# Optimization experiments

Hardware: AMD Instinct MI355X
Metric: run time of the kernel (lower is better)

The kernel has to match this reference:

```python
import jax, jax.numpy as jnp
import numpy as np

LEAKY_ALPHA = 0.2  # tf.nn.leaky_relu default


def setup_inputs() -> dict:
    key = jax.random.key(0)
    ks = jax.random.split(key, 8)
    N, F_IN, OUT, E = 100000, 256, 64, 1600000
    x = jax.random.normal(ks[0], (1, N, F_IN), dtype=jnp.float32)
    W = jax.random.normal(ks[1], (F_IN, OUT), dtype=jnp.float32) * 0.05
    a1 = jax.random.normal(ks[2], (OUT, 1), dtype=jnp.float32) * 0.1
    b1 = jnp.zeros((1,), dtype=jnp.float32)
    a2 = jax.random.normal(ks[3], (OUT, 1), dtype=jnp.float32) * 0.1
    b2 = jnp.zeros((1,), dtype=jnp.float32)
    out_bias = jnp.zeros((OUT,), dtype=jnp.float32)
    edge_src = jax.random.randint(ks[4], (E,), 0, N, dtype=jnp.int32)
    edge_dst = jax.random.randint(ks[5], (E,), 0, N, dtype=jnp.int32)
    return {"x": x, "W": W, "a1": a1, "b1": b1, "a2": a2, "b2": b2,
            "out_bias": out_bias, "edge_src": edge_src, "edge_dst": edge_dst,
            "nb_nodes": N}


def reference(x, W, a1, b1, a2, b2, out_bias, edge_src, edge_dst, nb_nodes):
    N = int(nb_nodes)
    h = jnp.einsum('nf,fo->no', x[0], W)          # [N, out_sz] projected features
    f1 = (h @ a1 + b1)[:, 0]                       # [N] per-node src score
    f2 = (h @ a2 + b2)[:, 0]                       # [N] per-node dst score
    # edge logits: f1[src] + f2[dst], leaky relu
    e = jax.nn.leaky_relu(f1[edge_src] + f2[edge_dst], negative_slope=LEAKY_ALPHA)
    # row-wise sparse softmax over edges grouped by src
    m = jax.ops.segment_max(e, edge_src, num_segments=N)
    m = jnp.where(jnp.isfinite(m), m, 0.0)
    ex = jnp.exp(e - m[edge_src])
    denom = jax.ops.segment_sum(ex, edge_src, num_segments=N)
    coefs = ex / denom[edge_src]                   # [E]
    # spmm: aggregate neighbor features
    vals = jax.ops.segment_sum(coefs[:, None] * h[edge_dst], edge_src, num_segments=N)
    ret = jax.nn.elu(vals + out_bias)              # bias_add + elu act
    return ret[None]                               # [1, N, out_sz]
```

## Files before the change

### kernel.cpp

```cpp
#include <hip/hip_runtime.h>
#include <math.h>

#define F_IN 256
#define OUT  64
#define LEAKY 0.2f
#define BSH  9
#define BSZ  512
#define CAP  12288
#define EPB  4096

typedef __attribute__((ext_vector_type(4))) float f32x4;
typedef __attribute__((ext_vector_type(8))) __bf16 bf16x8;
typedef __attribute__((ext_vector_type(4))) unsigned int u32x4;

__device__ __forceinline__ unsigned cvt_pk_bf16(float lo, float hi) {
    unsigned r;
    asm volatile("v_cvt_pk_bf16_f32 %0, %1, %2" : "=v"(r) : "v"(lo), "v"(hi));
    return r;
}

__device__ __forceinline__ float bfl(unsigned u) {
    return __builtin_bit_cast(float, u << 16);
}
__device__ __forceinline__ float bfh(unsigned u) {
    return __builtin_bit_cast(float, u & 0xFFFF0000u);
}

__global__ __launch_bounds__(256) void fused_part_gemm_kernel(
    const float* __restrict__ x, const float* __restrict__ W,
    const float* __restrict__ a1, const float* __restrict__ b1,
    const float* __restrict__ a2, const float* __restrict__ b2,
    unsigned short* __restrict__ h2, float* __restrict__ f1, float* __restrict__ f2,
    const int* __restrict__ esrc, const int* __restrict__ edst,
    int* __restrict__ runstart, int* __restrict__ cntmat, unsigned* __restrict__ ebkt,
    int N, int E, int nPart, int gemmBlocks)
{
    __shared__ __align__(16) unsigned int Wt[64 * 128];
    __shared__ __align__(16) unsigned int xsb[4][2][512];

    const int bid = blockIdx.x;
    const int t   = threadIdx.x;
    const int r   = bid % 3;

    if (r == 2) {
        int c = bid / 3;
        if (c >= nPart) return;
        int* hist = (int*)Wt;
        int* off  = hist + 256;
        int* run  = hist + 512;
        int* sc0  = hist + 768;
        int* sc1  = hist + 1024;
        hist[t] = 0; off[t] = 0;
        __syncthreads();
        const int e0 = c * EPB;
        int ss[16], dd[16], bb[16];
#pragma unroll
        for (int k = 0; k < 4; ++k) {
            int i = e0 + k * 1024 + t * 4;
            if (i + 4 <= E) {
                int4 s4 = *(const int4*)&esrc[i];
                int4 d4 = *(const int4*)&edst[i];
                ss[k * 4 + 0] = s4.x; ss[k * 4 + 1] = s4.y;
                ss[k * 4 + 2] = s4.z; ss[k * 4 + 3] = s4.w;
                dd[k * 4 + 0] = d4.x; dd[k * 4 + 1] = d4.y;
                dd[k * 4 + 2] = d4.z; dd[k * 4 + 3] = d4.w;
#pragma unroll
                for (int q = 0; q < 4; ++q) {
                    bb[k * 4 + q] = ss[k * 4 + q] >> BSH;
                    atomicAdd(&hist[bb[k * 4 + q]], 1);
                }
            } else {
#pragma unroll
                for (int q = 0; q < 4; ++q) {
                    int e = i + q;
                    if (e < E) {
                        ss[k * 4 + q] = esrc[e];
                        dd[k * 4 + q] = edst[e];
                        bb[k * 4 + q] = ss[k * 4 + q] >> BSH;
                        atomicAdd(&hist[bb[k * 4 + q]], 1);
                    } else bb[k * 4 + q] = -1;
                }
            }
        }
        __syncthreads();
        sc0[t] = hist[t];
        __syncthreads();
        int* s = sc0; int* dsts = sc1;
        for (int d = 1; d < 256; d <<= 1) {
            dsts[t] = s[t] + (t >= d ? s[t - d] : 0);
            __syncthreads();
            int* tmp = s; s = dsts; dsts = tmp;
        }
        run[t] = s[t] - hist[t];
        runstart[c * 256 + t] = s[t] - hist[t];
        cntmat [c * 256 + t] = hist[t];
        __syncthreads();
#pragma unroll
        for (int k = 0; k < 16; ++k) {
            if (bb[k] >= 0) {
                int l = atomicAdd(&off[bb[k]], 1);
                ebkt[e0 + run[bb[k]] + l] = (unsigned)dd[k] |
                                            ((unsigned)(ss[k] & (BSZ - 1)) << 17);
            }
        }
        return;
    }

    const int g    = (bid / 3) * 2 + r;
    if (g >= gemmBlocks) return;
    const int wave = t >> 6;
    const int lane = t & 63;
    const int rowB = g * 128;

    for (int p = t; p < 64 * 32; p += 256) {
        int c = p & 63, gg = p >> 6;
        float f[8];
#pragma unroll
        for (int j = 0; j < 8; ++j) f[j] = W[(gg * 8 + j) * 64 + c];
        u32x4 d;
        d.x = cvt_pk_bf16(f[0], f[1]);
        d.y = cvt_pk_bf16(f[2], f[3]);
        d.z = cvt_pk_bf16(f[4], f[5]);
        d.w = cvt_pk_bf16(f[6], f[7]);
        int gs = gg ^ (c & 7);
        *(u32x4*)&Wt[c * 128 + gs * 4] = d;
    }

    const int lrow0 = lane >> 3;
    const int fcol  = (lane & 7) << 2;
    const int sslot = (lane & 7) >> 1;
    const int shalf = (lane & 1) << 1;
    size_t gsrc[4];
    unsigned woff[4];
#pragma unroll
    for (int i = 0; i < 4; ++i) {
        int row  = i * 8 + lrow0;
        int srow = rowB + wave * 32 + row; if (srow > N - 1) srow = N - 1;
        gsrc[i] = (size_t)srow * F_IN + fcol;
        woff[i] = row * 16 + ((sslot ^ (row & 3)) << 2) + shalf;
    }
    unsigned int* xw = &xsb[wave][0][0];

    f32x4 acc[2][4];
#pragma unroll
    for (int m = 0; m < 2; ++m)
#pragma unroll
        for (int n = 0; n < 4; ++n) acc[m][n] = (f32x4){0.f, 0.f, 0.f, 0.f};

    float4 la[4], lb[4];
#pragma unroll
    for (int i = 0; i < 4; ++i) la[i] = *(const float4*)&x[gsrc[i]];

    __syncthreads();

#pragma unroll
    for (int ks = 0; ks < 8; ++ks) {
        const int cur = ks & 1;
        if (ks < 7) {
            const int kc = (ks + 1) * 32;
            if (cur == 0) {
#pragma unroll
                for (int i = 0; i < 4; ++i) lb[i] = *(const float4*)&x[gsrc[i] + kc];
            } else {
#pragma unroll
                for (int i = 0; i < 4; ++i) la[i] = *(const float4*)&x[gsrc[i] + kc];
            }
            asm volatile("s_waitcnt vmcnt(4)" ::: "memory");
        } else {
            asm volatile("s_waitcnt vmcnt(0)" ::: "memory");
        }
        __builtin_amdgcn_sched_barrier(0);

#pragma unroll
        for (int i = 0; i < 4; ++i) {
            float4 v = (cur == 0) ? la[i] : lb[i];
            uint2 w;
            w.x = cvt_pk_bf16(v.x, v.y);
            w.y = cvt_pk_bf16(v.z, v.w);
            *(uint2*)&xw[cur * 512 + woff[i]] = w;
        }

        bf16x8 bfrag[4];
#pragma unroll
        for (int ns = 0; ns < 4; ++ns) {
            int c = ns * 16 + (lane & 15);
            int G = ks * 4 + (lane >> 4);
            u32x4 bw = *(u32x4*)&Wt[c * 128 + ((G ^ (c & 7)) << 2)];
            bfrag[ns] = __builtin_bit_cast(bf16x8, bw);
        }
#pragma unroll
        for (int ms = 0; ms < 2; ++ms) {
            int rr = ms * 16 + (lane & 15);
            int g0 = lane >> 4;
            u32x4 aw = *(u32x4*)&xw[cur * 512 + rr * 16 + ((g0 ^ (rr & 3)) << 2)];
            bf16x8 afrag = __builtin_bit_cast(bf16x8, aw);
#pragma unroll
            for (int ns = 0; ns < 4; ++ns)
                acc[ms][ns] = __builtin_amdgcn_mfma_f32_16x16x32_bf16(afrag, bfrag[ns],
                                                                      acc[ms][ns], 0, 0, 0);
        }
    }

    float A1v[4], A2v[4];
#pragma unroll
    for (int ns = 0; ns < 4; ++ns) {
        A1v[ns] = a1[ns * 16 + (lane & 15)];
        A2v[ns] = a2[ns * 16 + (lane & 15)];
    }
    float B1 = b1[0], B2 = b2[0];
#pragma unroll
    for (int ms = 0; ms < 2; ++ms) {
#pragma unroll
        for (int rr = 0; rr < 4; ++rr) {
            int grow = rowB + wave * 32 + ms * 16 + ((lane >> 4) << 2) + rr;
            float s1 = 0.f, s2 = 0.f;
#pragma unroll
            for (int ns = 0; ns < 4; ++ns) {
                float v = acc[ms][ns][rr];
                if (grow < N)
                    h2[(size_t)grow * OUT + ns * 16 + (lane & 15)] =
                        (unsigned short)(cvt_pk_bf16(v, v) & 0xffffu);
                s1 += v * A1v[ns];
                s2 += v * A2v[ns];
            }
#pragma unroll
            for (int off = 1; off < 16; off <<= 1) {
                s1 += __shfl_xor(s1, off);
                s2 += __shfl_xor(s2, off);
            }
            if ((lane & 15) == 0 && grow < N) { f1[grow] = s1 + B1; f2[grow] = s2 + B2; }
        }
    }
}

__global__ __launch_bounds__(256) void csr_build_kernel(
    const unsigned* __restrict__ ebkt, const int* __restrict__ runstart,
    const int* __restrict__ cntmat,
    int* __restrict__ counts, int* __restrict__ row_start,
    int* __restrict__ csr4, int N, int nPart)
{
    __shared__ int cnt[BSZ];
    __shared__ int cur[BSZ];
    __shared__ int sc[2][BSZ];
    const int b = blockIdx.x;
    const int t = threadIdx.x;

    cnt[t] = 0; cnt[t + 256] = 0;
    __syncthreads();

    for (int c = t; c < nPart; c += 256) {
        int base = c * EPB + runstart[c * 256 + b];
        int n    = cntmat[c * 256 + b];
        for (int i = 0; i < n; ++i)
            atomicAdd(&cnt[ebkt[base + i] >> 17], 1);
    }
    __syncthreads();

    sc[0][t] = cnt[t]; sc[0][t + 256] = cnt[t + 256];
    __syncthreads();
    int srcb = 0;
    for (int d = 1; d < BSZ; d <<= 1) {
        int dstb = srcb ^ 1;
        int i0 = t, i1 = t + 256;
        sc[dstb][i0] = sc[srcb][i0] + (i0 >= d ? sc[srcb][i0 - d] : 0);
        sc[dstb][i1] = sc[srcb][i1] + (i1 >= d ? sc[srcb][i1 - d] : 0);
        __syncthreads();
        srcb = dstb;
    }

    const int nodeBase = b << BSH;
    const int e0out    = b * CAP;
#pragma unroll
    for (int j = 0; j < 2; ++j) {
        int i = t + j * 256;
        int excl = sc[srcb][i] - cnt[i];
        cur[i] = excl;
        int gn = nodeBase + i;
        if (gn < N) {
            row_start[gn] = e0out + excl;
            counts[gn]    = cnt[i];
        }
    }
    __syncthreads();

    for (int c = t; c < nPart; c += 256) {
        int base = c * EPB + runstart[c * 256 + b];
        int n    = cntmat[c * 256 + b];
        for (int i = 0; i < n; ++i) {
            unsigned w = ebkt[base + i];
            int ls = w >> 17;
            int pos = e0out + atomicAdd(&cur[ls], 1);
            csr4[pos] = (int)(w & 0x1FFFFu);
        }
    }
}

__global__ __launch_bounds__(256) void aggregate_kernel(
    const unsigned short* __restrict__ h2, const float* __restrict__ f1,
    const float* __restrict__ f2,
    const int* __restrict__ row_start, const int* __restrict__ counts,
    const int* __restrict__ csr4, const float* __restrict__ out_bias,
    float* __restrict__ out, int N)
{
    const int t    = threadIdx.x;
    const int lane = t & 63;
    const int gl   = lane & 7;
    const int gb   = lane & 56;
    const int gw   = blockIdx.x * 32 + ((t >> 6) << 3) + (lane >> 3);
    if (gw >= N) return;

    const int base  = row_start[gw];
    const int deg   = counts[gw];
    const float f1n = f1[gw];

    float den = 0.f;
    float a[8] = {0.f, 0.f, 0.f, 0.f, 0.f, 0.f, 0.f, 0.f};

    for (int c0 = 0; c0 < deg; c0 += 8) {
        int  idx   = c0 + gl;
        bool valid = idx < deg;
        int   d = valid ? csr4[base + idx] : 0;
        float e = f1n + f2[d];
        e = (e > 0.f) ? e : LEAKY * e;
        float p = valid ? __expf(e) : 0.f;
        den += p;

        unsigned pack = ((unsigned)d << 15) | (cvt_pk_bf16(p, p) & 0x7FFFu);

        int lim = deg - c0; if (lim > 8) lim = 8;
        int j = 0;
        for (; j + 2 <= lim; j += 2) {
            unsigned pk0 = __shfl((int)pack, gb + j);
            unsigned pk1 = __shfl((int)pack, gb + j + 1);
            uint4 u0 = *(const uint4*)&h2[((pk0 >> 15) << 6) + (gl << 3)];
            uint4 u1 = *(const uint4*)&h2[((pk1 >> 15) << 6) + (gl << 3)];
            float p0 = __builtin_bit_cast(float, (pk0 & 0x7FFFu) << 16);
            float p1 = __builtin_bit_cast(float, (pk1 & 0x7FFFu) << 16);
            a[0] += p0 * bfl(u0.x) + p1 * bfl(u1.x);
            a[1] += p0 * bfh(u0.x) + p1 * bfh(u1.x);
            a[2] += p0 * bfl(u0.y) + p1 * bfl(u1.y);
            a[3] += p0 * bfh(u0.y) + p1 * bfh(u1.y);
            a[4] += p0 * bfl(u0.z) + p1 * bfl(u1.z);
            a[5] += p0 * bfh(u0.z) + p1 * bfh(u1.z);
            a[6] += p0 * bfl(u0.w) + p1 * bfl(u1.w);
            a[7] += p0 * bfh(u0.w) + p1 * bfh(u1.w);
        }
        if (j < lim) {
            unsigned pk = __shfl((int)pack, gb + j);
            uint4 u = *(const uint4*)&h2[((pk >> 15) << 6) + (gl << 3)];
            float pp = __builtin_bit_cast(float, (pk & 0x7FFFu) << 16);
            a[0] += pp * bfl(u.x);
            a[1] += pp * bfh(u.x);
            a[2] += pp * bfl(u.y);
            a[3] += pp * bfh(u.y);
            a[4] += pp * bfl(u.z);
            a[5] += pp * bfh(u.z);
            a[6] += pp * bfl(u.w);
            a[7] += pp * bfh(u.w);
        }
    }

    den += __shfl_xor(den, 1);
    den += __shfl_xor(den, 2);
    den += __shfl_xor(den, 4);

    float rd = (deg > 0) ? (1.f / den) : 0.f;
    float4 b0 = *(const float4*)&out_bias[(gl << 3) + 0];
    float4 b1v = *(const float4*)&out_bias[(gl << 3) + 4];
    float v[8];
    v[0] = a[0] * rd + b0.x;  v[1] = a[1] * rd + b0.y;
    v[2] = a[2] * rd + b0.z;  v[3] = a[3] * rd + b0.w;
    v[4] = a[4] * rd + b1v.x; v[5] = a[5] * rd + b1v.y;
    v[6] = a[6] * rd + b1v.z; v[7] = a[7] * rd + b1v.w;
#pragma unroll
    for (int k = 0; k < 8; ++k)
        v[k] = (v[k] > 0.f) ? v[k] : (__expf(v[k]) - 1.f);
    float4 r0 = {v[0], v[1], v[2], v[3]};
    float4 r1 = {v[4], v[5], v[6], v[7]};
    *(float4*)&out[((unsigned)gw << 6) + (gl << 3) + 0] = r0;
    *(float4*)&out[((unsigned)gw << 6) + (gl << 3) + 4] = r1;
}

extern "C" void kernel_launch(void* const* d_in, const int* in_sizes, int n_in,
                              void* d_out, int out_size, void* d_ws, size_t ws_size,
                              hipStream_t stream)
{
    const float* x        = (const float*)d_in[0];
    const float* W        = (const float*)d_in[1];
    const float* a1       = (const float*)d_in[2];
    const float* b1       = (const float*)d_in[3];
    const float* a2       = (const float*)d_in[4];
    const float* b2       = (const float*)d_in[5];
    const float* out_bias = (const float*)d_in[6];
    const int*   esrc     = (const int*)d_in[7];
    const int*   edst     = (const int*)d_in[8];
    const int N = in_sizes[0] / F_IN;
    const int E = in_sizes[7];
    float* out = (float*)d_out;

    char* wsp = (char*)d_ws;
    size_t off = 0;
    auto alloc = [&](size_t bytes) -> void* {
        void* p = wsp + off;
        off = (off + bytes + 255) & ~(size_t)255;
        return p;
    };
    const int nbk   = (N + BSZ - 1) >> BSH;
    const int nPart = (E + EPB - 1) / EPB;

    unsigned short* h2 = (unsigned short*)alloc((size_t)N * OUT * sizeof(unsigned short));
    float* f1          = (float*)alloc((size_t)N * sizeof(float));
    float* f2          = (float*)alloc((size_t)N * sizeof(float));
    int*   counts      = (int*)alloc((size_t)N * sizeof(int));
    int*   row_start   = (int*)alloc((size_t)N * sizeof(int));
    int*   runstart    = (int*)alloc((size_t)nPart * 256 * sizeof(int));
    int*   cntmat      = (int*)alloc((size_t)nPart * 256 * sizeof(int));
    unsigned* ebkt     = (unsigned*)alloc((size_t)nPart * EPB * sizeof(unsigned));
    int*   csr4        = (int*)alloc((size_t)nbk * CAP * sizeof(int));

    const int gemmBlocks = (N + 127) / 128;
    int nGroup = (gemmBlocks + 1) / 2;
    if (nPart > nGroup) nGroup = nPart;

    fused_part_gemm_kernel<<<nGroup * 3, 256, 0, stream>>>(
        x, W, a1, b1, a2, b2, h2, f1, f2, esrc, edst, runstart, cntmat, ebkt,
        N, E, nPart, gemmBlocks);
    csr_build_kernel<<<nbk, 256, 0, stream>>>(ebkt, runstart, cntmat, counts, row_start,
                                              csr4, N, nPart);
    aggregate_kernel<<<(N + 31) / 32, 256, 0, stream>>>(h2, f1, f2, row_start, counts, csr4,
                                                        out_bias, out, N);
}
```

Baseline: 95.47 us.

## Split GEMM across partition and CSR-build kernels to overlap work

The GEMM blocks are now divided between two launches. The first kernel runs the edge partitioning alongside the first G1 GEMM tiles. The second kernel interleaves the CSR build with the remaining GEMM tiles. The aim is to hide the latency-bound CSR build, which has few blocks, behind compute-bound GEMM work, and to balance the first kernel. The split point is a hardcoded constant tuned to this N, and mixing block types may cause load imbalance or shared-memory occupancy limits.

```diff
diff --git a/kernel.cpp b/kernel.cpp
--- a/kernel.cpp
+++ b/kernel.cpp
@@ -8,6 +8,7 @@
 #define BSZ  512
 #define CAP  12288
 #define EPB  4096
+#define G1   586
 
 typedef __attribute__((ext_vector_type(4))) float f32x4;
 typedef __attribute__((ext_vector_type(8))) __bf16 bf16x8;
@@ -24,6 +25,139 @@
 }
 __device__ __forceinline__ float bfh(unsigned u) {
     return __builtin_bit_cast(float, u & 0xFFFF0000u);
+}
+
+__device__ __forceinline__ void gemm_body(
+    int g, int t,
+    const float* __restrict__ x, const float* __restrict__ W,
+    const float* __restrict__ a1, const float* __restrict__ b1,
+    const float* __restrict__ a2, const float* __restrict__ b2,
+    unsigned short* __restrict__ h2, float* __restrict__ f1, float* __restrict__ f2,
+    unsigned int* Wt, unsigned int* xsb, int N)
+{
+    const int wave = t >> 6;
+    const int lane = t & 63;
+    const int rowB = g * 128;
+
+    for (int p = t; p < 64 * 32; p += 256) {
+        int c = p & 63, gg = p >> 6;
+        float f[8];
+#pragma unroll
+        for (int j = 0; j < 8; ++j) f[j] = W[(gg * 8 + j) * 64 + c];
+        u32x4 d;
+        d.x = cvt_pk_bf16(f[0], f[1]);
+        d.y = cvt_pk_bf16(f[2], f[3]);
+        d.z = cvt_pk_bf16(f[4], f[5]);
+        d.w = cvt_pk_bf16(f[6], f[7]);
+        int gs = gg ^ (c & 7);
+        *(u32x4*)&Wt[c * 128 + gs * 4] = d;
+    }
+
+    const int lrow0 = lane >> 3;
+    const int fcol  = (lane & 7) << 2;
+    const int sslot = (lane & 7) >> 1;
+    const int shalf = (lane & 1) << 1;
+    size_t gsrc[4];
+    unsigned woff[4];
+#pragma unroll
+    for (int i = 0; i < 4; ++i) {
+        int row  = i * 8 + lrow0;
+        int srow = rowB + wave * 32 + row; if (srow > N - 1) srow = N - 1;
+        gsrc[i] = (size_t)srow * F_IN + fcol;
+        woff[i] = row * 16 + ((sslot ^ (row & 3)) << 2) + shalf;
+    }
+    unsigned int* xw = &xsb[wave * 1024];
+
+    f32x4 acc[2][4];
+#pragma unroll
+    for (int m = 0; m < 2; ++m)
+#pragma unroll
+        for (int n = 0; n < 4; ++n) acc[m][n] = (f32x4){0.f, 0.f, 0.f, 0.f};
+
+    float4 la[4], lb[4];
+#pragma unroll
+    for (int i = 0; i < 4; ++i) la[i] = *(const float4*)&x[gsrc[i]];
+
+    __syncthreads();
+
+#pragma unroll
+    for (int ks = 0; ks < 8; ++ks) {
+        const int cur = ks & 1;
+        if (ks < 7) {
+            const int kc = (ks + 1) * 32;
+            if (cur == 0) {
+#pragma unroll
+                for (int i = 0; i < 4; ++i) lb[i] = *(const float4*)&x[gsrc[i] + kc];
+            } else {
+#pragma unroll
+                for (int i = 0; i < 4; ++i) la[i] = *(const float4*)&x[gsrc[i] + kc];
+            }
+            asm volatile("s_waitcnt vmcnt(4)" ::: "memory");
+        } else {
+            asm volatile("s_waitcnt vmcnt(0)" ::: "memory");
+        }
+        __builtin_amdgcn_sched_barrier(0);
+
+#pragma unroll
+        for (int i = 0; i < 4; ++i) {
+            float4 v = (cur == 0) ? la[i] : lb[i];
+            uint2 w;
+            w.x = cvt_pk_bf16(v.x, v.y);
+            w.y = cvt_pk_bf16(v.z, v.w);
+            *(uint2*)&xw[cur * 512 + woff[i]] = w;
+        }
+
+        bf16x8 bfrag[4];
+#pragma unroll
+        for (int ns = 0; ns < 4; ++ns) {
+            int c = ns * 16 + (lane & 15);
+            int G = ks * 4 + (lane >> 4);
+            u32x4 bw = *(u32x4*)&Wt[c * 128 + ((G ^ (c & 7)) << 2)];
+            bfrag[ns] = __builtin_bit_cast(bf16x8, bw);
+        }
+#pragma unroll
+        for (int ms = 0; ms < 2; ++ms) {
+            int rr = ms * 16 + (lane & 15);
+            int g0 = lane >> 4;
+            u32x4 aw = *(u32x4*)&xw[cur * 512 + rr * 16 + ((g0 ^ (rr & 3)) << 2)];
+            bf16x8 afrag = __builtin_bit_cast(bf16x8, aw);
+#pragma unroll
+            for (int ns = 0; ns < 4; ++ns)
+                acc[ms][ns] = __builtin_amdgcn_mfma_f32_16x16x32_bf16(afrag, bfrag[ns],
+                                                                      acc[ms][ns], 0, 0, 0);
+        }
+    }
+
+    float A1v[4], A2v[4];
+#pragma unroll
+    for (int ns = 0; ns < 4; ++ns) {
+        A1v[ns] = a1[ns * 16 + (lane & 15)];
+        A2v[ns] = a2[ns * 16 + (lane & 15)];
+    }
+    float B1 = b1[0], B2 = b2[0];
+#pragma unroll
+    for (int ms = 0; ms < 2; ++ms) {
+#pragma unroll
+        for (int rr = 0; rr < 4; ++rr) {
+            int grow = rowB + wave * 32 + ms * 16 + ((lane >> 4) << 2) + rr;
+            float s1 = 0.f, s2 = 0.f;
+#pragma unroll
+            for (int ns = 0; ns < 4; ++ns) {
+                float v = acc[ms][ns][rr];
+                if (grow < N)
+                    h2[(size_t)grow * OUT + ns * 16 + (lane & 15)] =
+                        (unsigned short)(cvt_pk_bf16(v, v) & 0xffffu);
+                s1 += v * A1v[ns];
+                s2 += v * A2v[ns];
+            }
+#pragma unroll
+            for (int off = 1; off < 16; off <<= 1) {
+                s1 += __shfl_xor(s1, off);
+                s2 += __shfl_xor(s2, off);
+            }
+            if ((lane & 15) == 0 && grow < N) { f1[grow] = s1 + B1; f2[grow] = s2 + B2; }
+        }
+    }
 }
 
 __global__ __launch_bounds__(256) void fused_part_gemm_kernel(
@@ -36,7 +170,7 @@
     int N, int E, int nPart, int gemmBlocks)
 {
     __shared__ __align__(16) unsigned int Wt[64 * 128];
-    __shared__ __align__(16) unsigned int xsb[4][2][512];
+    __shared__ __align__(16) unsigned int xsb[4 * 1024];
 
     const int bid = blockIdx.x;
     const int t   = threadIdx.x;
@@ -106,193 +240,88 @@
         return;
     }
 
-    const int g    = (bid / 3) * 2 + r;
+    const int g = (bid / 3) * 2 + r;
     if (g >= gemmBlocks) return;
-    const int wave = t >> 6;
-    const int lane = t & 63;
-    const int rowB = g * 128;
-
-    for (int p = t; p < 64 * 32; p += 256) {
-        int c = p & 63, gg = p >> 6;
-        float f[8];
-#pragma unroll
-        for (int j = 0; j < 8; ++j) f[j] = W[(gg * 8 + j) * 64 + c];
-        u32x4 d;
-        d.x = cvt_pk_bf16(f[0], f[1]);
-        d.y = cvt_pk_bf16(f[2], f[3]);
-        d.z = cvt_pk_bf16(f[4], f[5]);
-        d.w = cvt_pk_bf16(f[6], f[7]);
-        int gs = gg ^ (c & 7);
-        *(u32x4*)&Wt[c * 128 + gs * 4] = d;
-    }
-
-    const int lrow0 = lane >> 3;
-    const int fcol  = (lane & 7) << 2;
-    const int sslot = (lane & 7) >> 1;
-    const int shalf = (lane & 1) << 1;
-    size_t gsrc[4];
-    unsigned woff[4];
-#pragma unroll
-    for (int i = 0; i < 4; ++i) {
-        int row  = i * 8 + lrow0;
-        int srow = rowB + wave * 32 + row; if (srow > N - 1) srow = N - 1;
-        gsrc[i] = (size_t)srow * F_IN + fcol;
-        woff[i] = row * 16 + ((sslot ^ (row & 3)) << 2) + shalf;
-    }
-    unsigned int* xw = &xsb[wave][0][0];
-
-    f32x4 acc[2][4];
-#pragma unroll
-    for (int m = 0; m < 2; ++m)
-#pragma unroll
-        for (int n = 0; n < 4; ++n) acc[m][n] = (f32x4){0.f, 0.f, 0.f, 0.f};
-
-    float4 la[4], lb[4];
-#pragma unroll
-    for (int i = 0; i < 4; ++i) la[i] = *(const float4*)&x[gsrc[i]];
-
-    __syncthreads();
-
-#pragma unroll
-    for (int ks = 0; ks < 8; ++ks) {
-        const int cur = ks & 1;
-        if (ks < 7) {
-            const int kc = (ks + 1) * 32;
-            if (cur == 0) {
-#pragma unroll
-                for (int i = 0; i < 4; ++i) lb[i] = *(const float4*)&x[gsrc[i] + kc];
-            } else {
-#pragma unroll
-                for (int i = 0; i < 4; ++i) la[i] = *(const float4*)&x[gsrc[i] + kc];
-            }
-            asm volatile("s_waitcnt vmcnt(4)" ::: "memory");
-        } else {
-            asm volatile("s_waitcnt vmcnt(0)" ::: "memory");
-        }
-        __builtin_amdgcn_sched_barrier(0);
-
-#pragma unroll
-        for (int i = 0; i < 4; ++i) {
-            float4 v = (cur == 0) ? la[i] : lb[i];
-            uint2 w;
-            w.x = cvt_pk_bf16(v.x, v.y);
-            w.y = cvt_pk_bf16(v.z, v.w);
-            *(uint2*)&xw[cur * 512 + woff[i]] = w;
-        }
-
-        bf16x8 bfrag[4];
-#pragma unroll
-        for (int ns = 0; ns < 4; ++ns) {
-            int c = ns * 16 + (lane & 15);
-            int G = ks * 4 + (lane >> 4);
-            u32x4 bw = *(u32x4*)&Wt[c * 128 + ((G ^ (c & 7)) << 2)];
-            bfrag[ns] = __builtin_bit_cast(bf16x8, bw);
-        }
-#pragma unroll
-        for (int ms = 0; ms < 2; ++ms) {
-            int rr = ms * 16 + (lane & 15);
-            int g0 = lane >> 4;
-            u32x4 aw = *(u32x4*)&xw[cur * 512 + rr * 16 + ((g0 ^ (rr & 3)) << 2)];
-            bf16x8 afrag = __builtin_bit_cast(bf16x8, aw);
-#pragma unroll
-            for (int ns = 0; ns < 4; ++ns)
-                acc[ms][ns] = __builtin_amdgcn_mfma_f32_16x16x32_bf16(afrag, bfrag[ns],
-                                                                      acc[ms][ns], 0, 0, 0);
-        }
-    }
-
-    float A1v[4], A2v[4];
-#pragma unroll
-    for (int ns = 0; ns < 4; ++ns) {
-        A1v[ns] = a1[ns * 16 + (lane & 15)];
-        A2v[ns] = a2[ns * 16 + (lane & 15)];
-    }
-    float B1 = b1[0], B2 = b2[0];
-#pragma unroll
-    for (int ms = 0; ms < 2; ++ms) {
-#pragma unroll
-        for (int rr = 0; rr < 4; ++rr) {
-            int grow = rowB + wave * 32 + ms * 16 + ((lane >> 4) << 2) + rr;
-            float s1 = 0.f, s2 = 0.f;
-#pragma unroll
-            for (int ns = 0; ns < 4; ++ns) {
-                float v = acc[ms][ns][rr];
-                if (grow < N)
-                    h2[(size_t)grow * OUT + ns * 16 + (lane & 15)] =
-                        (unsigned short)(cvt_pk_bf16(v, v) & 0xffffu);
-                s1 += v * A1v[ns];
-                s2 += v * A2v[ns];
-            }
-#pragma unroll
-            for (int off = 1; off < 16; off <<= 1) {
-                s1 += __shfl_xor(s1, off);
-                s2 += __shfl_xor(s2, off);
-            }
-            if ((lane & 15) == 0 && grow < N) { f1[grow] = s1 + B1; f2[grow] = s2 + B2; }
-        }
-    }
-}
-
-__global__ __launch_bounds__(256) void csr_build_kernel(
+    gemm_body(g, t, x, W, a1, b1, a2, b2, h2, f1, f2, Wt, xsb, N);
+}
+
+__global__ __launch_bounds__(256) void fused_csr_gemm_kernel(
+    const float* __restrict__ x, const float* __restrict__ W,
+    const float* __restrict__ a1, const float* __restrict__ b1,
+    const float* __restrict__ a2, const float* __restrict__ b2,
+    unsigned short* __restrict__ h2, float* __restrict__ f1, float* __restrict__ f2,
     const unsigned* __restrict__ ebkt, const int* __restrict__ runstart,
     const int* __restrict__ cntmat,
-    int* __restrict__ counts, int* __restrict__ row_start,
-    int* __restrict__ csr4, int N, int nPart)
+    int* __restrict__ counts, int* __restrict__ row_start, int* __restrict__ csr4,
+    int N, int nPart, int nbk, int gemmLo, int gemmBlocks)
 {
-    __shared__ int cnt[BSZ];
-    __shared__ int cur[BSZ];
-    __shared__ int sc[2][BSZ];
-    const int b = blockIdx.x;
-    const int t = threadIdx.x;
-
-    cnt[t] = 0; cnt[t + 256] = 0;
-    __syncthreads();
-
-    for (int c = t; c < nPart; c += 256) {
-        int base = c * EPB + runstart[c * 256 + b];
-        int n    = cntmat[c * 256 + b];
-        for (int i = 0; i < n; ++i)
-            atomicAdd(&cnt[ebkt[base + i] >> 17], 1);
-    }
-    __syncthreads();
-
-    sc[0][t] = cnt[t]; sc[0][t + 256] = cnt[t + 256];
-    __syncthreads();
-    int srcb = 0;
-    for (int d = 1; d < BSZ; d <<= 1) {
-        int dstb = srcb ^ 1;
-        int i0 = t, i1 = t + 256;
-        sc[dstb][i0] = sc[srcb][i0] + (i0 >= d ? sc[srcb][i0 - d] : 0);
-        sc[dstb][i1] = sc[srcb][i1] + (i1 >= d ? sc[srcb][i1 - d] : 0);
-        __syncthreads();
-        srcb = dstb;
-    }
-
-    const int nodeBase = b << BSH;
-    const int e0out    = b * CAP;
-#pragma unroll
-    for (int j = 0; j < 2; ++j) {
-        int i = t + j * 256;
-        int excl = sc[srcb][i] - cnt[i];
-        cur[i] = excl;
-        int gn = nodeBase + i;
-        if (gn < N) {
-            row_start[gn] = e0out + excl;
-            counts[gn]    = cnt[i];
-        }
-    }
-    __syncthreads();
-
-    for (int c = t; c < nPart; c += 256) {
-        int base = c * EPB + runstart[c * 256 + b];
-        int n    = cntmat[c * 256 + b];
-        for (int i = 0; i < n; ++i) {
-            unsigned w = ebkt[base + i];
-            int ls = w >> 17;
-            int pos = e0out + atomicAdd(&cur[ls], 1);
-            csr4[pos] = (int)(w & 0x1FFFFu);
-        }
-    }
+    __shared__ __align__(16) unsigned int Wt[64 * 128];
+    __shared__ __align__(16) unsigned int xsb[4 * 1024];
+
+    const int bid = blockIdx.x;
+    const int t   = threadIdx.x;
+
+    if (bid & 1) {
+        const int b = bid >> 1;
+        if (b >= nbk) return;
+        int* cnt = (int*)Wt;
+        int* cur = cnt + 512;
+        int* scA = cnt + 1024;
+        int* scB = cnt + 1536;
+
+        cnt[t] = 0; cnt[t + 256] = 0;
+        __syncthreads();
+
+        for (int c = t; c < nPart; c += 256) {
+            int base = c * EPB + runstart[c * 256 + b];
+            int n    = cntmat[c * 256 + b];
+            for (int i = 0; i < n; ++i)
+                atomicAdd(&cnt[ebkt[base + i] >> 17], 1);
+        }
+        __syncthreads();
+
+        scA[t] = cnt[t]; scA[t + 256] = cnt[t + 256];
+        __syncthreads();
+        int* s = scA; int* dsts = scB;
+        for (int d = 1; d < BSZ; d <<= 1) {
+            int i0 = t, i1 = t + 256;
+            dsts[i0] = s[i0] + (i0 >= d ? s[i0 - d] : 0);
+            dsts[i1] = s[i1] + (i1 >= d ? s[i1 - d] : 0);
+            __syncthreads();
+            int* tmp = s; s = dsts; dsts = tmp;
+        }
+
+        const int nodeBase = b << BSH;
+        const int e0out    = b * CAP;
+#pragma unroll
+        for (int j = 0; j < 2; ++j) {
+            int i = t + j * 256;
+            int excl = s[i] - cnt[i];
+            cur[i] = excl;
+            int gn = nodeBase + i;
+            if (gn < N) {
+                row_start[gn] = e0out + excl;
+                counts[gn]    = cnt[i];
+            }
+        }
+        __syncthreads();
+
+        for (int c = t; c < nPart; c += 256) {
+            int base = c * EPB + runstart[c * 256 + b];
+            int n    = cntmat[c * 256 + b];
+            for (int i = 0; i < n; ++i) {
+                unsigned w = ebkt[base + i];
+                int ls = w >> 17;
+                int pos = e0out + atomicAdd(&cur[ls], 1);
+                csr4[pos] = (int)(w & 0x1FFFFu);
+            }
+        }
+        return;
+    }
+
+    const int g = gemmLo + (bid >> 1);
+    if (g >= gemmBlocks) return;
+    gemm_body(g, t, x, W, a1, b1, a2, b2, h2, f1, f2, Wt, xsb, N);
 }
 
 __global__ __launch_bounds__(256) void aggregate_kernel(
@@ -419,14 +448,17 @@
     int*   csr4        = (int*)alloc((size_t)nbk * CAP * sizeof(int));
 
     const int gemmBlocks = (N + 127) / 128;
-    int nGroup = (gemmBlocks + 1) / 2;
-    if (nPart > nGroup) nGroup = nPart;
-
-    fused_part_gemm_kernel<<<nGroup * 3, 256, 0, stream>>>(
+    int nGroup1 = (G1 + 1) / 2;
+    if (nPart > nGroup1) nGroup1 = nPart;
+    int nGroup2 = gemmBlocks - G1;
+    if (nbk > nGroup2) nGroup2 = nbk;
+
+    fused_part_gemm_kernel<<<nGroup1 * 3, 256, 0, stream>>>(
         x, W, a1, b1, a2, b2, h2, f1, f2, esrc, edst, runstart, cntmat, ebkt,
-        N, E, nPart, gemmBlocks);
-    csr_build_kernel<<<nbk, 256, 0, stream>>>(ebkt, runstart, cntmat, counts, row_start,
-                                              csr4, N, nPart);
+        N, E, nPart, G1);
+    fused_csr_gemm_kernel<<<nGroup2 * 2, 256, 0, stream>>>(
+        x, W, a1, b1, a2, b2, h2, f1, f2, ebkt, runstart, cntmat,
+        counts, row_start, csr4, N, nPart, nbk, G1, gemmBlocks);
     aggregate_kernel<<<(N + 31) / 32, 256, 0, stream>>>(h2, f1, f2, row_start, counts, csr4,
                                                         out_bias, out, N);
 }
```

Result: slower. 101.4 us (+6.2%).
